# Optimization experiments

Measured on AMD Instinct MI355X. Metric: run time of the kernel, lower is better.

## Reference

```python
import jax, jax.numpy as jnp
import numpy as np

N = 50000      # nodes
E = 800000     # edges (before self-loops)
F_IN = 128     # input features
HID = 64       # hidden width
CLS = 40       # classes
NEG_SLOPE = 0.2  # PyG GATConv default
EPS = 1e-16


def setup_inputs() -> dict:
    key = jax.random.key(0)
    ks = jax.random.split(key, 16)

    def lin(k, fi, fo):
        return jax.random.normal(k, (fi, fo), jnp.float32) / np.float32(np.sqrt(fi))

    def att(k, f):
        return jax.random.normal(k, (f,), jnp.float32) / np.float32(np.sqrt(f))

    return {
        "x": jax.random.normal(ks[0], (N, F_IN), jnp.float32),
        "edge_index": jax.random.randint(ks[1], (2, E), 0, N, dtype=jnp.int64),
        "W1": lin(ks[2], F_IN, HID), "a_src1": att(ks[3], HID), "a_dst1": att(ks[4], HID), "b1": jnp.zeros((HID,), jnp.float32),
        "W2": lin(ks[5], HID, HID),  "a_src2": att(ks[6], HID), "a_dst2": att(ks[7], HID), "b2": jnp.zeros((HID,), jnp.float32),
        "W3": lin(ks[8], HID, CLS),  "a_src3": att(ks[9], CLS), "a_dst3": att(ks[10], CLS), "b3": jnp.zeros((CLS,), jnp.float32),
    }


def gat_layer(x, src, dst, W, a_src, a_dst, b, n):
    # Single-head GATConv (PyG semantics, heads=1, add_self_loops already applied).
    h = x @ W                                  # [n, out]
    s_src = h @ a_src                          # [n]
    s_dst = h @ a_dst                          # [n]
    e = jax.nn.leaky_relu(s_src[src] + s_dst[dst], NEG_SLOPE)  # [E']
    # softmax over incoming edges of each destination node
    m = jax.ops.segment_max(e, dst, num_segments=n)            # [n]
    e = jnp.exp(e - m[dst])
    denom = jax.ops.segment_sum(e, dst, num_segments=n)        # [n]
    alpha = e / (denom[dst] + EPS)                             # [E']
    out = jax.ops.segment_sum(h[src] * alpha[:, None], dst, num_segments=n)
    return out + b


def reference(x, edge_index, W1, a_src1, a_dst1, b1, W2, a_src2, a_dst2, b2, W3, a_src3, a_dst3, b3):
    n = x.shape[0]
    loop = jnp.arange(n, dtype=edge_index.dtype)
    src = jnp.concatenate([edge_index[0], loop])   # add self-loops (GATConv default)
    dst = jnp.concatenate([edge_index[1], loop])

    h = gat_layer(x, src, dst, W1, a_src1, a_dst1, b1, n)
    h = jax.nn.gelu(h, approximate=False)          # torch F.gelu default = exact erf
    h = gat_layer(h, src, dst, W2, a_src2, a_dst2, b2, n)
    h = jax.nn.gelu(h, approximate=False)
    out = gat_layer(h, src, dst, W3, a_src3, a_dst3, b3, n)
    return out
```

## Files before the change

kernel.cpp:

```cpp
#include <hip/hip_runtime.h>
#include <hip/hip_bf16.h>
#include <math.h>


#define PAD_CAP 64

__device__ __forceinline__ int detect64(const int* __restrict__ ei) {
  int any = 0;
#pragma unroll
  for (int i = 1; i < 64; i += 2) any |= ei[i];
  return any == 0;
}

__device__ __forceinline__ void load_edge(const int* __restrict__ ei, int E,
                                          int e, int is64, int n, int& s,
                                          int& d) {
  if (is64) {
    s = ei[2 * e];
    d = ei[2 * (E + e)];
  } else {
    s = ei[e];
    d = ei[E + e];
  }
  s = min(max(s, 0), n - 1);
  d = min(max(d, 0), n - 1);
}

__global__ void scatter_padded(const int* __restrict__ ei, int E, int n,
                               int* __restrict__ deg, int* __restrict__ col) {
  const int is64 = detect64(ei);
  const int e = blockIdx.x * blockDim.x + threadIdx.x;
  if (e >= E + n) return;
  int s, d;
  if (e < E) load_edge(ei, E, e, is64, n, s, d);
  else s = d = e - E;
  const int pos = atomicAdd(deg + d, 1);
  if (pos < PAD_CAP) col[((size_t)d << 6) + pos] = s;
}


template <int F_IN, int F_OUT>
__global__ __launch_bounds__(256) void gemm_att(
    const float* __restrict__ x, const float* __restrict__ W,
    const float* __restrict__ a_src, const float* __restrict__ a_dst,
    __hip_bfloat16* __restrict__ h, float* __restrict__ s_src,
    float* __restrict__ s_dst, int n) {
  constexpr int TF = F_OUT / 4;
  __shared__ float Xt[F_IN * 65];
  __shared__ float red[2][4][64];
  const int wave = threadIdx.x >> 6, lane = threadIdx.x & 63;
  const int nb0 = blockIdx.x * 64;
  const int node = nb0 + lane;

  {
    constexpr int Q = F_IN / 4;
    for (int i = threadIdx.x; i < 64 * Q; i += 256) {
      const int nd = i / Q, k4 = i % Q;
      float4 v = {0.f, 0.f, 0.f, 0.f};
      if (nb0 + nd < n)
        v = *(const float4*)(x + (size_t)(nb0 + nd) * F_IN + 4 * k4);
      Xt[(4 * k4 + 0) * 65 + nd] = v.x;
      Xt[(4 * k4 + 1) * 65 + nd] = v.y;
      Xt[(4 * k4 + 2) * 65 + nd] = v.z;
      Xt[(4 * k4 + 3) * 65 + nd] = v.w;
    }
  }
  __syncthreads();

  const int f0 = __builtin_amdgcn_readfirstlane(wave * TF);
  float acc[TF];
#pragma unroll
  for (int ff = 0; ff < TF; ++ff) acc[ff] = 0.f;

#pragma unroll 4
  for (int k = 0; k < F_IN; ++k) {
    const float xk = Xt[k * 65 + lane];
#pragma unroll
    for (int ff = 0; ff < TF; ++ff)
      acc[ff] = fmaf(xk, W[k * F_OUT + f0 + ff], acc[ff]);
  }

  float pa = 0.f, pb = 0.f;
#pragma unroll
  for (int ff = 0; ff < TF; ++ff) {
    pa = fmaf(acc[ff], a_src[f0 + ff], pa);
    pb = fmaf(acc[ff], a_dst[f0 + ff], pb);
  }
  if (node < n) {
#pragma unroll
    for (int ff = 0; ff < TF; ++ff)
      h[(size_t)node * F_OUT + f0 + ff] = __float2bfloat16(acc[ff]);
  }
  red[0][wave][lane] = pa;
  red[1][wave][lane] = pb;
  __syncthreads();
  if (wave == 0 && node < n) {
    s_src[node] = red[0][0][lane] + red[0][1][lane] + red[0][2][lane] +
                  red[0][3][lane];
    s_dst[node] = red[1][0][lane] + red[1][1][lane] + red[1][2][lane] +
                  red[1][3][lane];
  }
}

template <int F_OUT, bool GELU>
__global__ __launch_bounds__(256) void attn_aggr(
    const int* __restrict__ col, const int* __restrict__ deg_arr,
    const float* __restrict__ ssrc, const float* __restrict__ sdst,
    const __hip_bfloat16* __restrict__ h, const float* __restrict__ bias,
    float* __restrict__ out, int n) {
  const int wave = threadIdx.x >> 6, lane = threadIdx.x & 63;
  const int d = blockIdx.x * 4 + wave;
  if (d >= n) return;
  const int beg = d << 6;
  const int deg = min(deg_arr[d], PAD_CAP);
  const float sd = sdst[d];

  int s0 = 0;
  float v0 = 0.f, m = -INFINITY;
  if (lane < deg) {
    s0 = col[beg + lane];
    float t = ssrc[s0] + sd;
    v0 = t > 0.f ? t : 0.2f * t;
    m = v0;
  }
#pragma unroll
  for (int off = 32; off > 0; off >>= 1) m = fmaxf(m, __shfl_xor(m, off));

  const float w0 = (lane < deg) ? __expf(v0 - m) : 0.f;
  float den = w0;
#pragma unroll
  for (int off = 32; off > 0; off >>= 1) den += __shfl_xor(den, off);
  const float inv = 1.f / (den + 1e-16f);

  const __hip_bfloat16* hl = h + lane;
  float acc = 0.f;
  const int dmain = deg;
  int i = 0;
  for (; i + 16 <= dmain; i += 16) {
    int ss[16];
    float ww[16], hh[16];
#pragma unroll
    for (int j = 0; j < 16; ++j) {
      ss[j] = __shfl(s0, i + j);
      ww[j] = __shfl(w0, i + j);
    }
    if (lane < F_OUT) {
#pragma unroll
      for (int j = 0; j < 16; ++j)
        hh[j] = __bfloat162float(hl[(size_t)ss[j] * F_OUT]);
    } else {
#pragma unroll
      for (int j = 0; j < 16; ++j) hh[j] = 0.f;
    }
#pragma unroll
    for (int j = 0; j < 16; ++j) acc = fmaf(ww[j], hh[j], acc);
  }
  for (; i + 4 <= dmain; i += 4) {
    int ss[4];
    float ww[4], hh[4];
#pragma unroll
    for (int j = 0; j < 4; ++j) {
      ss[j] = __shfl(s0, i + j);
      ww[j] = __shfl(w0, i + j);
    }
    if (lane < F_OUT) {
#pragma unroll
      for (int j = 0; j < 4; ++j)
        hh[j] = __bfloat162float(hl[(size_t)ss[j] * F_OUT]);
    } else {
#pragma unroll
      for (int j = 0; j < 4; ++j) hh[j] = 0.f;
    }
#pragma unroll
    for (int j = 0; j < 4; ++j) acc = fmaf(ww[j], hh[j], acc);
  }
  for (; i < dmain; ++i) {
    const int s = __shfl(s0, i);
    const float wi = __shfl(w0, i);
    if (lane < F_OUT)
      acc = fmaf(wi, __bfloat162float(hl[(size_t)s * F_OUT]), acc);
  }

  if (lane < F_OUT) {
    float v = acc * inv + bias[lane];
    if (GELU) v = 0.5f * v * (1.0f + erff(v * 0.70710678118654752f));
    out[(size_t)d * F_OUT + lane] = v;
  }
}

extern "C" void kernel_launch(void* const* d_in, const int* in_sizes, int n_in,
                              void* d_out, int out_size, void* d_ws,
                              size_t ws_size, hipStream_t stream) {
  const float* x = (const float*)d_in[0];
  const int* ei = (const int*)d_in[1];
  const float* W1 = (const float*)d_in[2];
  const float* as1 = (const float*)d_in[3];
  const float* ad1 = (const float*)d_in[4];
  const float* b1 = (const float*)d_in[5];
  const float* W2 = (const float*)d_in[6];
  const float* as2 = (const float*)d_in[7];
  const float* ad2 = (const float*)d_in[8];
  const float* b2 = (const float*)d_in[9];
  const float* W3 = (const float*)d_in[10];
  const float* as3 = (const float*)d_in[11];
  const float* ad3 = (const float*)d_in[12];
  const float* b3 = (const float*)d_in[13];

  const int n = in_sizes[0] / 128;
  const int E = in_sizes[1] / 2;
  const int total = E + n;

  const size_t need = ((size_t)n * (32 + 64 + 1 + 1 + 1 + PAD_CAP)) * 4 + 256;
  if (ws_size < need) return;

  __hip_bfloat16* hb = (__hip_bfloat16*)d_ws;
  float* B = (float*)d_ws + (size_t)n * 32;
  float* ssrc = B + (size_t)n * 64;
  float* sdst = ssrc + n;
  int* deg = (int*)(sdst + n);
  int* col = deg + n;

  const int tb = (total + 255) / 256;
  const int gemm_blocks = (n + 63) / 64;
  const int aggr_blocks = (n + 3) / 4;

  hipMemsetAsync(deg, 0, (size_t)n * 4, stream);
  scatter_padded<<<tb, 256, 0, stream>>>(ei, E, n, deg, col);

  gemm_att<128, 64><<<gemm_blocks, 256, 0, stream>>>(x, W1, as1, ad1, hb, ssrc,
                                                     sdst, n);
  attn_aggr<64, true><<<aggr_blocks, 256, 0, stream>>>(col, deg, ssrc, sdst,
                                                       hb, b1, B, n);

  gemm_att<64, 64><<<gemm_blocks, 256, 0, stream>>>(B, W2, as2, ad2, hb, ssrc,
                                                    sdst, n);
  attn_aggr<64, true><<<aggr_blocks, 256, 0, stream>>>(col, deg, ssrc, sdst,
                                                       hb, b2, B, n);

  gemm_att<64, 40><<<gemm_blocks, 256, 0, stream>>>(B, W3, as3, ad3, hb, ssrc,
                                                    sdst, n);
  attn_aggr<40, false><<<aggr_blocks, 256, 0, stream>>>(
      col, deg, ssrc, sdst, hb, b3, (float*)d_out, n);
}
```

Before: 308.6 us.

## Fuse attention aggregation with next layer's GEMM and score computation

Layers 1 and 2 now run their aggregation (softmax-weighted gather, bias, GELU) directly into a shared-memory tile. The next layer's linear transform and attention-score dot products are computed from that tile in the same kernel. This removes the fp32 intermediate round trip through global memory and two kernel launches, and ping-pongs between two bf16 feature buffers. The cost is fewer waves in flight during the gather phase: each wave processes 16 nodes serially in 64-node blocks, which may reduce latency hiding for the random gathers.

```diff
diff --git a/kernel.cpp b/kernel.cpp
--- a/kernel.cpp
+++ b/kernel.cpp
@@ -36,6 +36,69 @@
   else s = d = e - E;
   const int pos = atomicAdd(deg + d, 1);
   if (pos < PAD_CAP) col[((size_t)d << 6) + pos] = s;
+}
+
+
+__device__ __forceinline__ float aggr_one(
+    const int* __restrict__ col, const int* __restrict__ deg_arr,
+    const float* __restrict__ ssrc, float sd,
+    const __hip_bfloat16* __restrict__ hl , int d, int lane) {
+  const int beg = d << 6;
+  const int deg = min(deg_arr[d], PAD_CAP);
+
+  int s0 = 0;
+  float v0 = 0.f, m = -INFINITY;
+  if (lane < deg) {
+    s0 = col[beg + lane];
+    float t = ssrc[s0] + sd;
+    v0 = t > 0.f ? t : 0.2f * t;
+    m = v0;
+  }
+#pragma unroll
+  for (int off = 32; off > 0; off >>= 1) m = fmaxf(m, __shfl_xor(m, off));
+
+  const float w0 = (lane < deg) ? __expf(v0 - m) : 0.f;
+  float den = w0;
+#pragma unroll
+  for (int off = 32; off > 0; off >>= 1) den += __shfl_xor(den, off);
+  const float inv = 1.f / (den + 1e-16f);
+
+  float acc = 0.f;
+  int i = 0;
+  for (; i + 16 <= deg; i += 16) {
+    int ss[16];
+    float ww[16], hh[16];
+#pragma unroll
+    for (int j = 0; j < 16; ++j) {
+      ss[j] = __shfl(s0, i + j);
+      ww[j] = __shfl(w0, i + j);
+    }
+#pragma unroll
+    for (int j = 0; j < 16; ++j)
+      hh[j] = __bfloat162float(hl[(size_t)ss[j] * 64]);
+#pragma unroll
+    for (int j = 0; j < 16; ++j) acc = fmaf(ww[j], hh[j], acc);
+  }
+  for (; i + 4 <= deg; i += 4) {
+    int ss[4];
+    float ww[4], hh[4];
+#pragma unroll
+    for (int j = 0; j < 4; ++j) {
+      ss[j] = __shfl(s0, i + j);
+      ww[j] = __shfl(w0, i + j);
+    }
+#pragma unroll
+    for (int j = 0; j < 4; ++j)
+      hh[j] = __bfloat162float(hl[(size_t)ss[j] * 64]);
+#pragma unroll
+    for (int j = 0; j < 4; ++j) acc = fmaf(ww[j], hh[j], acc);
+  }
+  for (; i < deg; ++i) {
+    const int s = __shfl(s0, i);
+    const float wi = __shfl(w0, i);
+    acc = fmaf(wi, __bfloat162float(hl[(size_t)s * 64]), acc);
+  }
+  return acc * inv;
 }
 
 
@@ -71,7 +134,6 @@
   float acc[TF];
 #pragma unroll
   for (int ff = 0; ff < TF; ++ff) acc[ff] = 0.f;
-
 #pragma unroll 4
   for (int k = 0; k < F_IN; ++k) {
     const float xk = Xt[k * 65 + lane];
@@ -102,8 +164,73 @@
   }
 }
 
-template <int F_OUT, bool GELU>
-__global__ __launch_bounds__(256) void attn_aggr(
+template <int F_OUT>
+__global__ __launch_bounds__(256) void aggr_gemm(
+    const int* __restrict__ col, const int* __restrict__ deg_arr,
+    const float* __restrict__ ssrc_p, const float* __restrict__ sdst_p,
+    const __hip_bfloat16* __restrict__ h_p, const float* __restrict__ bias_p,
+    const float* __restrict__ W, const float* __restrict__ a_src,
+    const float* __restrict__ a_dst, __hip_bfloat16* __restrict__ h_n,
+    float* __restrict__ ssrc_n, float* __restrict__ sdst_n, int n) {
+  constexpr int F_IN = 64;
+  constexpr int TF = F_OUT / 4;
+  __shared__ float Xt[F_IN * 65];
+  __shared__ float red[2][4][64];
+  const int wave = threadIdx.x >> 6, lane = threadIdx.x & 63;
+  const int nb0 = blockIdx.x * 64;
+  const int node = nb0 + lane;
+
+  const __hip_bfloat16* hl = h_p + lane;
+#pragma unroll 1
+  for (int j = 0; j < 16; ++j) {
+    const int nd = wave * 16 + j;
+    const int d = nb0 + nd;
+    float v = 0.f;
+    if (d < n) {
+      v = aggr_one(col, deg_arr, ssrc_p, sdst_p[d], hl, d, lane) +
+          bias_p[lane];
+      v = 0.5f * v * (1.0f + erff(v * 0.70710678118654752f));
+    }
+    Xt[lane * 65 + nd] = v;
+  }
+  __syncthreads();
+
+  const int f0 = __builtin_amdgcn_readfirstlane(wave * TF);
+  float acc[TF];
+#pragma unroll
+  for (int ff = 0; ff < TF; ++ff) acc[ff] = 0.f;
+#pragma unroll 4
+  for (int k = 0; k < F_IN; ++k) {
+    const float xk = Xt[k * 65 + lane];
+#pragma unroll
+    for (int ff = 0; ff < TF; ++ff)
+      acc[ff] = fmaf(xk, W[k * F_OUT + f0 + ff], acc[ff]);
+  }
+
+  float pa = 0.f, pb = 0.f;
+#pragma unroll
+  for (int ff = 0; ff < TF; ++ff) {
+    pa = fmaf(acc[ff], a_src[f0 + ff], pa);
+    pb = fmaf(acc[ff], a_dst[f0 + ff], pb);
+  }
+  if (node < n) {
+#pragma unroll
+    for (int ff = 0; ff < TF; ++ff)
+      h_n[(size_t)node * F_OUT + f0 + ff] = __float2bfloat16(acc[ff]);
+  }
+  red[0][wave][lane] = pa;
+  red[1][wave][lane] = pb;
+  __syncthreads();
+  if (wave == 0 && node < n) {
+    ssrc_n[node] = red[0][0][lane] + red[0][1][lane] + red[0][2][lane] +
+                   red[0][3][lane];
+    sdst_n[node] = red[1][0][lane] + red[1][1][lane] + red[1][2][lane] +
+                   red[1][3][lane];
+  }
+}
+
+template <int F_OUT>
+__global__ __launch_bounds__(256) void attn_aggr_out(
     const int* __restrict__ col, const int* __restrict__ deg_arr,
     const float* __restrict__ ssrc, const float* __restrict__ sdst,
     const __hip_bfloat16* __restrict__ h, const float* __restrict__ bias,
@@ -125,7 +252,6 @@
   }
 #pragma unroll
   for (int off = 32; off > 0; off >>= 1) m = fmaxf(m, __shfl_xor(m, off));
-
   const float w0 = (lane < deg) ? __expf(v0 - m) : 0.f;
   float den = w0;
 #pragma unroll
@@ -134,9 +260,8 @@
 
   const __hip_bfloat16* hl = h + lane;
   float acc = 0.f;
-  const int dmain = deg;
   int i = 0;
-  for (; i + 16 <= dmain; i += 16) {
+  for (; i + 16 <= deg; i += 16) {
     int ss[16];
     float ww[16], hh[16];
 #pragma unroll
@@ -155,7 +280,7 @@
 #pragma unroll
     for (int j = 0; j < 16; ++j) acc = fmaf(ww[j], hh[j], acc);
   }
-  for (; i + 4 <= dmain; i += 4) {
+  for (; i + 4 <= deg; i += 4) {
     int ss[4];
     float ww[4], hh[4];
 #pragma unroll
@@ -174,18 +299,15 @@
 #pragma unroll
     for (int j = 0; j < 4; ++j) acc = fmaf(ww[j], hh[j], acc);
   }
-  for (; i < dmain; ++i) {
+  for (; i < deg; ++i) {
     const int s = __shfl(s0, i);
     const float wi = __shfl(w0, i);
     if (lane < F_OUT)
       acc = fmaf(wi, __bfloat162float(hl[(size_t)s * F_OUT]), acc);
   }
 
-  if (lane < F_OUT) {
-    float v = acc * inv + bias[lane];
-    if (GELU) v = 0.5f * v * (1.0f + erff(v * 0.70710678118654752f));
-    out[(size_t)d * F_OUT + lane] = v;
-  }
+  if (lane < F_OUT)
+    out[(size_t)d * F_OUT + lane] = acc * inv + bias[lane];
 }
 
 extern "C" void kernel_launch(void* const* d_in, const int* in_sizes, int n_in,
@@ -210,14 +332,14 @@
   const int E = in_sizes[1] / 2;
   const int total = E + n;
 
-  const size_t need = ((size_t)n * (32 + 64 + 1 + 1 + 1 + PAD_CAP)) * 4 + 256;
+  const size_t need = ((size_t)n * (32 + 32 + 2 + 2 + 1 + PAD_CAP)) * 4 + 256;
   if (ws_size < need) return;
 
-  __hip_bfloat16* hb = (__hip_bfloat16*)d_ws;
-  float* B = (float*)d_ws + (size_t)n * 32;
-  float* ssrc = B + (size_t)n * 64;
-  float* sdst = ssrc + n;
-  int* deg = (int*)(sdst + n);
+  __hip_bfloat16* hA = (__hip_bfloat16*)d_ws;
+  __hip_bfloat16* hB = hA + (size_t)n * 64;
+  float* sA = (float*)d_ws + (size_t)n * 64;
+  float* sB = sA + 2 * (size_t)n;
+  int* deg = (int*)(sB + 2 * (size_t)n);
   int* col = deg + n;
 
   const int tb = (total + 255) / 256;
@@ -227,18 +349,12 @@
   hipMemsetAsync(deg, 0, (size_t)n * 4, stream);
   scatter_padded<<<tb, 256, 0, stream>>>(ei, E, n, deg, col);
 
-  gemm_att<128, 64><<<gemm_blocks, 256, 0, stream>>>(x, W1, as1, ad1, hb, ssrc,
-                                                     sdst, n);
-  attn_aggr<64, true><<<aggr_blocks, 256, 0, stream>>>(col, deg, ssrc, sdst,
-                                                       hb, b1, B, n);
-
-  gemm_att<64, 64><<<gemm_blocks, 256, 0, stream>>>(B, W2, as2, ad2, hb, ssrc,
-                                                    sdst, n);
-  attn_aggr<64, true><<<aggr_blocks, 256, 0, stream>>>(col, deg, ssrc, sdst,
-                                                       hb, b2, B, n);
-
-  gemm_att<64, 40><<<gemm_blocks, 256, 0, stream>>>(B, W3, as3, ad3, hb, ssrc,
-                                                    sdst, n);
-  attn_aggr<40, false><<<aggr_blocks, 256, 0, stream>>>(
-      col, deg, ssrc, sdst, hb, b3, (float*)d_out, n);
-}
+  gemm_att<128, 64><<<gemm_blocks, 256, 0, stream>>>(x, W1, as1, ad1, hA, sA,
+                                                     sA + n, n);
+  aggr_gemm<64><<<gemm_blocks, 256, 0, stream>>>(
+      col, deg, sA, sA + n, hA, b1, W2, as2, ad2, hB, sB, sB + n, n);
+  aggr_gemm<40><<<gemm_blocks, 256, 0, stream>>>(
+      col, deg, sB, sB + n, hB, b2, W3, as3, ad3, hA, sA, sA + n, n);
+  attn_aggr_out<40><<<aggr_blocks, 256, 0, stream>>>(col, deg, sA, sA + n, hA,
+                                                     b3, (float*)d_out, n);
+}
```

Result: slower. 332.5 us (+7.7%).
